# Performance work log

Hardware: AMD Instinct MI355X
Metric: run time of the kernel (lower is better)

## Reference

```python
import jax, jax.numpy as jnp
import numpy as np

B, T, C = 4, 2048, 1024
N_HEAD = 16
HEAD_DIM = C // N_HEAD


def setup_inputs() -> dict:
    key = jax.random.key(0)
    ks = jax.random.split(key, 5)
    s = 0.02
    return {
        "x": jax.random.normal(ks[0], (B, T, C), dtype=jnp.float32),
        "w_attn": jax.random.normal(ks[1], (C, 3 * C), dtype=jnp.float32) * s,
        "b_attn": jnp.zeros((3 * C,), dtype=jnp.float32),
        "w_proj": jax.random.normal(ks[2], (C, C), dtype=jnp.float32) * s,
        "b_proj": jnp.zeros((C,), dtype=jnp.float32),
    }


def reference(x, w_attn, b_attn, w_proj, b_proj):
    Bx, Tx, Cx = x.shape
    qkv = x @ w_attn + b_attn  # [B,T,3C]
    q, k, v = jnp.split(qkv, 3, axis=-1)
    # [B, H, T, D]
    q = q.reshape(Bx, Tx, N_HEAD, HEAD_DIM).transpose(0, 2, 1, 3)
    k = k.reshape(Bx, Tx, N_HEAD, HEAD_DIM).transpose(0, 2, 1, 3)
    v = v.reshape(Bx, Tx, N_HEAD, HEAD_DIM).transpose(0, 2, 1, 3)
    scale = 1.0 / np.sqrt(HEAD_DIM).astype(np.float32)
    att = jnp.einsum("bhqd,bhkd->bhqk", q, k) * scale  # [B,H,T,T]
    causal = jnp.tril(jnp.ones((Tx, Tx), dtype=bool))
    att = jnp.where(causal[None, None], att, jnp.float32(-jnp.inf))
    att = jax.nn.softmax(att, axis=-1)
    y = jnp.einsum("bhqk,bhkd->bhqd", att, v)  # [B,H,T,D]
    y = y.transpose(0, 2, 1, 3).reshape(Bx, Tx, Cx)
    return y @ w_proj + b_proj
```

## Files before the change

kernel.cpp:

```cpp
#include <hip/hip_runtime.h>
#include <hip/hip_bf16.h>

#define T_SEQ 2048
#define NHEAD 16
#define HDIM  64
#define CDIM  1024

typedef __attribute__((ext_vector_type(8))) short bf16x8;
typedef __attribute__((ext_vector_type(4))) short bf16x4;
typedef __attribute__((ext_vector_type(4))) float f32x4;

__device__ __forceinline__ unsigned short f2bf(float f) {
  union { __hip_bfloat16 h; unsigned short u; } c;
  c.h = __float2bfloat16(f);
  return c.u;
}

#define GLD16(g, l) __builtin_amdgcn_global_load_lds( \
  (const __attribute__((address_space(1))) void*)(g), \
  (__attribute__((address_space(3))) void*)(l), 16, 0, 0)

__global__ void prep_all(const float* __restrict__ x, const float* __restrict__ wa,
                         const float* __restrict__ wp, unsigned short* __restrict__ xb,
                         unsigned short* __restrict__ wat, unsigned short* __restrict__ wpt) {
  __shared__ float tile[32][33];
  const int bid = blockIdx.x;
  if (bid < 8192) {
    const int i = bid * 256 + threadIdx.x;
    const float4 v = ((const float4*)x)[i];
    ushort4 o;
    o.x = f2bf(v.x); o.y = f2bf(v.y); o.z = f2bf(v.z); o.w = f2bf(v.w);
    ((ushort4*)xb)[i] = o;
    return;
  }
  const float* in; unsigned short* out; int R, C, bx, by;
  if (bid < 11264) { in = wa; out = wat; R = 1024; C = 3072; bx = (bid - 8192) % 96; by = (bid - 8192) / 96; }
  else             { in = wp; out = wpt; R = 1024; C = 1024; bx = (bid - 11264) % 32; by = (bid - 11264) / 32; }
  const int tx = threadIdx.x & 31, ty = threadIdx.x >> 5;
  const int c0 = bx * 32, r0 = by * 32;
#pragma unroll
  for (int i = 0; i < 32; i += 8)
    tile[ty + i][tx] = in[(size_t)(r0 + ty + i) * C + c0 + tx];
  __syncthreads();
#pragma unroll
  for (int i = 0; i < 32; i += 8)
    out[(size_t)(c0 + ty + i) * R + r0 + tx] = f2bf(tile[tx][ty + i]);
}

template<int OUTF32>
__global__ __launch_bounds__(256, 2)
void gemm_bt(const unsigned short* __restrict__ A, const unsigned short* __restrict__ BT,
             const float* __restrict__ bias, void* __restrict__ outp,
             int M, int N, int K) {
  const int tid = threadIdx.x;
  const int w = tid >> 6, lane = tid & 63;
  const int lg = lane >> 4, l15 = lane & 15;
  const int wr = w >> 1, wc = w & 1;

  const int nb = gridDim.x * gridDim.y;
  const int fid = blockIdx.y * gridDim.x + blockIdx.x;
  const int swz = (fid & 7) * (nb >> 3) + (fid >> 3);
  const int n0 = (swz % gridDim.x) * 128, m0 = (swz / gridDim.x) * 128;

  __shared__ unsigned short As[128 * 64];
  __shared__ unsigned short Bs[128 * 64];

  f32x4 acc[4][4] = {};

  for (int k0 = 0; k0 < K; k0 += 64) {
    __syncthreads();
#pragma unroll
    for (int i = 0; i < 4; ++i) {
      const int cb = i * 256 + w * 64;
      const int c  = cb + lane;
      const int row = c >> 3, s = c & 7;
      const int sg = s ^ (row & 7);
      GLD16(A  + (size_t)(m0 + row) * K + k0 + sg * 8, (char*)As + cb * 16);
      GLD16(BT + (size_t)(n0 + row) * K + k0 + sg * 8, (char*)Bs + cb * 16);
    }
    __syncthreads();
#pragma unroll
    for (int ks = 0; ks < 2; ++ks) {
      bf16x8 af[4], bfr[4];
#pragma unroll
      for (int mt = 0; mt < 4; ++mt) {
        const int row = wr * 64 + mt * 16 + l15;
        af[mt] = *(const bf16x8*)&As[row * 64 + (((ks * 4 + lg) ^ (l15 & 7)) << 3)];
      }
#pragma unroll
      for (int nt = 0; nt < 4; ++nt) {
        const int row = wc * 64 + nt * 16 + l15;
        bfr[nt] = *(const bf16x8*)&Bs[row * 64 + (((ks * 4 + lg) ^ (l15 & 7)) << 3)];
      }
#pragma unroll
      for (int mt = 0; mt < 4; ++mt)
#pragma unroll
        for (int nt = 0; nt < 4; ++nt)
          acc[mt][nt] = __builtin_amdgcn_mfma_f32_16x16x32_bf16(af[mt], bfr[nt], acc[mt][nt], 0, 0, 0);
    }
  }

#pragma unroll
  for (int mt = 0; mt < 4; ++mt) {
#pragma unroll
    for (int nt = 0; nt < 4; ++nt) {
      const int col = n0 + wc * 64 + nt * 16 + l15;
      const float bv = bias[col];
#pragma unroll
      for (int j = 0; j < 4; ++j) {
        const int row = m0 + wr * 64 + mt * 16 + lg * 4 + j;
        const float v = acc[mt][nt][j] + bv;
        if (OUTF32) ((float*)outp)[(size_t)row * N + col] = v;
        else ((unsigned short*)outp)[(size_t)row * N + col] = f2bf(v);
      }
    }
  }
}

#define EXPC 0.18033688f
__global__ __launch_bounds__(512, 4)
void attn_causal5(const unsigned short* __restrict__ qkv, unsigned short* __restrict__ att) {
  const int tid = threadIdx.x;
  const int w = tid >> 6, lane = tid & 63;
  const int lg = lane >> 4, l15 = lane & 15;

  const int fid = blockIdx.x;
  const int f2 = (fid & 7) * 64 + (fid >> 3);
  const int pair = f2 & 7, bh = f2 >> 3;
  const int b = bh >> 4, h = bh & 15;

  __shared__ unsigned short Kl[2][2][64][32];
  __shared__ unsigned short Vt[2][64][64];

  const unsigned short* base = qkv + (size_t)b * T_SEQ * 3072;

  auto STAGE_K = [&](int kv0, int buf) {
    const int c = tid;
    const int kc = c >> 8, slot = (c >> 2) & 63;
    const int s2 = (c & 3) ^ ((slot >> 1) & 3);
    const int v = (slot & 35) | ((slot & 8) << 1) | ((slot & 4) << 1) | ((slot & 16) >> 2);
    GLD16(base + (size_t)(kv0 + v) * 3072 + 1024 + h * 64 + kc * 32 + s2 * 8,
          (char*)&Kl[buf][0][0][0] + w * 1024);
  };

  bf16x4 vra, vrb;
  const int vkp = tid >> 4, vd4 = tid & 15;
  auto VLOAD = [&](int kv0) {
    const unsigned short* p = base + (size_t)(kv0 + 2 * vkp) * 3072 + 2048 + h * 64 + vd4 * 4;
    vra = *(const bf16x4*)p;
    vrb = *(const bf16x4*)(p + 3072);
  };
  auto VWRITE = [&](int buf) {
    const int ch = vkp >> 2, cl = (vkp & 3) * 2;
#pragma unroll
    for (int j = 0; j < 4; ++j) {
      const int r = vd4 * 4 + j;
      const unsigned int u = (unsigned short)vra[j] |
                             ((unsigned int)(unsigned short)vrb[j] << 16);
      *(unsigned int*)&Vt[buf][r][((ch ^ (r >> 3) ^ (r & 7)) << 3) + cl] = u;
    }
  };

  bf16x8 ones;
#pragma unroll
  for (int j = 0; j < 8; ++j) ones[j] = (short)0x3F80;

  for (int half = 0; half < 2; ++half) {
    const int qt = half ? (15 - pair) : pair;
    const int q0 = qt << 7;
    const int ntl = (qt + 1) << 1;
    const int qminS = __builtin_amdgcn_readfirstlane(q0 + w * 16);
    const int qme = qminS + l15;

    bf16x8 qf[2];
#pragma unroll
    for (int kc = 0; kc < 2; ++kc)
      qf[kc] = *(const bf16x8*)(base + (size_t)qme * 3072 + h * 64 + kc * 32 + lg * 8);

    f32x4 oacc[4] = {};
    f32x4 lsum = {};
    float m = -1e30f;

    STAGE_K(0, 0);
    VLOAD(0);
    VWRITE(0);
    __syncthreads();

    for (int t = 0; t < ntl; ++t) {
      const int cur = t & 1, nxt = cur ^ 1;
      const bool pf = (t + 1) < ntl;
      if (pf) { STAGE_K((t + 1) << 6, nxt); VLOAD((t + 1) << 6); }
      const int kv0 = t << 6;

      if (kv0 <= qminS + 15) {
        const int ksl = (lg ^ ((l15 >> 1) & 3)) * 8;
        f32x4 sc[4];
        __builtin_amdgcn_s_setprio(1);
#pragma unroll
        for (int kg = 0; kg < 4; ++kg) {
          f32x4 s = {};
#pragma unroll
          for (int kc = 0; kc < 2; ++kc) {
            bf16x8 kf = *(const bf16x8*)&Kl[cur][kc][kg * 16 + l15][ksl];
            s = __builtin_amdgcn_mfma_f32_16x16x32_bf16(kf, qf[kc], s, 0, 0, 0);
          }
          sc[kg] = s;
        }
        __builtin_amdgcn_s_setprio(0);

        float sv[4][4];
        if (kv0 + 63 > qminS) {
#pragma unroll
          for (int kg = 0; kg < 4; ++kg) {
            const int colb = kv0 + ((kg >> 1) << 5) + ((kg & 1) << 2) + lg * 8;
#pragma unroll
            for (int j = 0; j < 4; ++j)
              sv[kg][j] = (colb + j <= qme) ? sc[kg][j] : -1e30f;
          }
        } else {
#pragma unroll
          for (int kg = 0; kg < 4; ++kg)
#pragma unroll
            for (int j = 0; j < 4; ++j) sv[kg][j] = sc[kg][j];
        }

        float mx = -1e30f;
#pragma unroll
        for (int kg = 0; kg < 4; ++kg) {
          const float a = fmaxf(sv[kg][0], sv[kg][1]);
          const float c2 = fmaxf(sv[kg][2], sv[kg][3]);
          mx = fmaxf(mx, fmaxf(a, c2));
        }

        if (__any(mx > m + 55.4f)) {
          float mw = fmaxf(mx, __shfl_xor(mx, 16));
          mw = fmaxf(mw, __shfl_xor(mw, 32));
          const float mnew = fmaxf(m, mw);
          const float alc = exp2f((m - mnew) * EXPC);
          m = mnew;
          float alq[4];
#pragma unroll
          for (int j = 0; j < 4; ++j)
            alq[j] = __shfl(alc, (lane & 48) | (lg * 4 + j));
#pragma unroll
          for (int j = 0; j < 4; ++j) {
            lsum[j] *= alq[j];
#pragma unroll
            for (int dt = 0; dt < 4; ++dt) oacc[dt][j] *= alq[j];
          }
        }

        const float mc = m * EXPC;
        bf16x8 pa[2];
#pragma unroll
        for (int kg = 0; kg < 4; ++kg) {
          const int ks = kg >> 1, off = (kg & 1) * 4;
#pragma unroll
          for (int j = 0; j < 4; ++j) {
            const float p = exp2f(__fmaf_rn(sv[kg][j], EXPC, -mc));
            pa[ks][off + j] = (short)f2bf(p);
          }
        }

        __builtin_amdgcn_s_setprio(1);
        lsum = __builtin_amdgcn_mfma_f32_16x16x32_bf16(pa[0], ones, lsum, 0, 0, 0);
        lsum = __builtin_amdgcn_mfma_f32_16x16x32_bf16(pa[1], ones, lsum, 0, 0, 0);
#pragma unroll
        for (int dt = 0; dt < 4; ++dt) {
          f32x4 o = oacc[dt];
          const int d = dt * 16 + l15;
          const int gx = (d >> 3) ^ (d & 7);
#pragma unroll
          for (int ks = 0; ks < 2; ++ks) {
            bf16x8 vb = *(const bf16x8*)&Vt[cur][d][((ks * 4 + lg) ^ gx) << 3];
            o = __builtin_amdgcn_mfma_f32_16x16x32_bf16(pa[ks], vb, o, 0, 0, 0);
          }
          oacc[dt] = o;
        }
        __builtin_amdgcn_s_setprio(0);
      }

      if (pf) VWRITE(nxt);
      __syncthreads();
    }

    f32x4 inv;
#pragma unroll
    for (int j = 0; j < 4; ++j) inv[j] = __builtin_amdgcn_rcpf(lsum[j]);
#pragma unroll
    for (int dt = 0; dt < 4; ++dt)
#pragma unroll
      for (int j = 0; j < 4; ++j) {
        const int q = qminS + lg * 4 + j;
        att[(size_t)(b * T_SEQ + q) * CDIM + h * HDIM + dt * 16 + l15] =
            f2bf(oacc[dt][j] * inv[j]);
      }
  }
}

extern "C" void kernel_launch(void* const* d_in, const int* in_sizes, int n_in,
                              void* d_out, int out_size, void* d_ws, size_t ws_size,
                              hipStream_t stream) {
  const float* x      = (const float*)d_in[0];
  const float* w_attn = (const float*)d_in[1];
  const float* b_attn = (const float*)d_in[2];
  const float* w_proj = (const float*)d_in[3];
  const float* b_proj = (const float*)d_in[4];

  char* ws = (char*)d_ws;
  unsigned short* xb  = (unsigned short*)(ws + 0);
  unsigned short* wat = (unsigned short*)(ws + 16777216);
  unsigned short* wpt = (unsigned short*)(ws + 23068672);
  unsigned short* qkv = (unsigned short*)(ws + 25165824);
  unsigned short* att = (unsigned short*)(ws + 75497472);

  prep_all<<<dim3(12288), 256, 0, stream>>>(x, w_attn, w_proj, xb, wat, wpt);
  gemm_bt<0><<<dim3(24, 64), 256, 0, stream>>>(xb, wat, b_attn, (void*)qkv, 8192, 3072, 1024);
  attn_causal5<<<dim3(512), 512, 0, stream>>>(qkv, att);
  gemm_bt<1><<<dim3(8, 64), 256, 0, stream>>>(att, wpt, b_proj, d_out, 8192, 1024, 1024);
}
```

Before: 172.4 us.

## Fuse x-to-bf16 conversion into QKV GEMM and process both causal tiles together

The separate pass that converted x from fp32 to bf16 is removed. The QKV GEMM now reads fp32 activations directly, converts them in registers and stores them into the swizzled LDS tile, so the intermediate bf16 buffer is never written or read back. The attention kernel now walks the KV sequence once for both its low and high query tiles, reusing each staged K/V block for two sets of MFMAs instead of running two separate passes. The cost is that A-tile loading moves from async global-to-LDS copies to synchronous register loads with twice the bytes, and the attention kernel needs more registers for two sets of accumulators.

```diff
diff --git a/kernel.cpp b/kernel.cpp
--- a/kernel.cpp
+++ b/kernel.cpp
@@ -20,22 +20,13 @@
   (const __attribute__((address_space(1))) void*)(g), \
   (__attribute__((address_space(3))) void*)(l), 16, 0, 0)
 
-__global__ void prep_all(const float* __restrict__ x, const float* __restrict__ wa,
-                         const float* __restrict__ wp, unsigned short* __restrict__ xb,
+__global__ void prep_all(const float* __restrict__ wa, const float* __restrict__ wp,
                          unsigned short* __restrict__ wat, unsigned short* __restrict__ wpt) {
   __shared__ float tile[32][33];
   const int bid = blockIdx.x;
-  if (bid < 8192) {
-    const int i = bid * 256 + threadIdx.x;
-    const float4 v = ((const float4*)x)[i];
-    ushort4 o;
-    o.x = f2bf(v.x); o.y = f2bf(v.y); o.z = f2bf(v.z); o.w = f2bf(v.w);
-    ((ushort4*)xb)[i] = o;
-    return;
-  }
   const float* in; unsigned short* out; int R, C, bx, by;
-  if (bid < 11264) { in = wa; out = wat; R = 1024; C = 3072; bx = (bid - 8192) % 96; by = (bid - 8192) / 96; }
-  else             { in = wp; out = wpt; R = 1024; C = 1024; bx = (bid - 11264) % 32; by = (bid - 11264) / 32; }
+  if (bid < 3072) { in = wa; out = wat; R = 1024; C = 3072; bx = bid % 96; by = bid / 96; }
+  else            { in = wp; out = wpt; R = 1024; C = 1024; bx = (bid - 3072) % 32; by = (bid - 3072) / 32; }
   const int tx = threadIdx.x & 31, ty = threadIdx.x >> 5;
   const int c0 = bx * 32, r0 = by * 32;
 #pragma unroll
@@ -47,9 +38,9 @@
     out[(size_t)(c0 + ty + i) * R + r0 + tx] = f2bf(tile[tx][ty + i]);
 }
 
-template<int OUTF32>
+template<int OUTF32, int AF32>
 __global__ __launch_bounds__(256, 2)
-void gemm_bt(const unsigned short* __restrict__ A, const unsigned short* __restrict__ BT,
+void gemm_bt(const void* __restrict__ Ap, const unsigned short* __restrict__ BT,
              const float* __restrict__ bias, void* __restrict__ outp,
              int M, int N, int K) {
   const int tid = threadIdx.x;
@@ -75,7 +66,21 @@
       const int c  = cb + lane;
       const int row = c >> 3, s = c & 7;
       const int sg = s ^ (row & 7);
-      GLD16(A  + (size_t)(m0 + row) * K + k0 + sg * 8, (char*)As + cb * 16);
+      if (AF32) {
+        const float* A32 = (const float*)Ap;
+        const float* p = A32 + (size_t)(m0 + row) * K + k0 + sg * 8;
+        const float4 f0 = *(const float4*)p;
+        const float4 f1 = *(const float4*)(p + 4);
+        bf16x8 pk;
+        pk[0] = (short)f2bf(f0.x); pk[1] = (short)f2bf(f0.y);
+        pk[2] = (short)f2bf(f0.z); pk[3] = (short)f2bf(f0.w);
+        pk[4] = (short)f2bf(f1.x); pk[5] = (short)f2bf(f1.y);
+        pk[6] = (short)f2bf(f1.z); pk[7] = (short)f2bf(f1.w);
+        *(bf16x8*)&As[row * 64 + s * 8] = pk;
+      } else {
+        const unsigned short* A16 = (const unsigned short*)Ap;
+        GLD16(A16 + (size_t)(m0 + row) * K + k0 + sg * 8, (char*)As + cb * 16);
+      }
       GLD16(BT + (size_t)(n0 + row) * K + k0 + sg * 8, (char*)Bs + cb * 16);
     }
     __syncthreads();
@@ -119,7 +124,7 @@
 
 #define EXPC 0.18033688f
 __global__ __launch_bounds__(512, 4)
-void attn_causal5(const unsigned short* __restrict__ qkv, unsigned short* __restrict__ att) {
+void attn_causal11(const unsigned short* __restrict__ qkv, unsigned short* __restrict__ att) {
   const int tid = threadIdx.x;
   const int w = tid >> 6, lane = tid & 63;
   const int lg = lane >> 4, l15 = lane & 15;
@@ -128,6 +133,7 @@
   const int f2 = (fid & 7) * 64 + (fid >> 3);
   const int pair = f2 & 7, bh = f2 >> 3;
   const int b = bh >> 4, h = bh & 15;
+  const int lo = pair, hi = 15 - pair;
 
   __shared__ unsigned short Kl[2][2][64][32];
   __shared__ unsigned short Vt[2][64][64];
@@ -165,135 +171,220 @@
 #pragma unroll
   for (int j = 0; j < 8; ++j) ones[j] = (short)0x3F80;
 
-  for (int half = 0; half < 2; ++half) {
-    const int qt = half ? (15 - pair) : pair;
-    const int q0 = qt << 7;
-    const int ntl = (qt + 1) << 1;
-    const int qminS = __builtin_amdgcn_readfirstlane(q0 + w * 16);
-    const int qme = qminS + l15;
-
-    bf16x8 qf[2];
-#pragma unroll
-    for (int kc = 0; kc < 2; ++kc)
-      qf[kc] = *(const bf16x8*)(base + (size_t)qme * 3072 + h * 64 + kc * 32 + lg * 8);
-
-    f32x4 oacc[4] = {};
-    f32x4 lsum = {};
-    float m = -1e30f;
-
-    STAGE_K(0, 0);
-    VLOAD(0);
-    VWRITE(0);
+  const int ntl = (hi + 1) << 1;
+  const int qminA = __builtin_amdgcn_readfirstlane(lo * 128 + w * 16);
+  const int qminB = __builtin_amdgcn_readfirstlane(hi * 128 + w * 16);
+  const int qmeA = qminA + l15, qmeB = qminB + l15;
+
+  bf16x8 qfA[2], qfB[2];
+#pragma unroll
+  for (int kc = 0; kc < 2; ++kc) {
+    qfA[kc] = *(const bf16x8*)(base + (size_t)qmeA * 3072 + h * 64 + kc * 32 + lg * 8);
+    qfB[kc] = *(const bf16x8*)(base + (size_t)qmeB * 3072 + h * 64 + kc * 32 + lg * 8);
+  }
+
+  f32x4 oaccA[4] = {}, oaccB[4] = {};
+  f32x4 lsumA = {}, lsumB = {};
+  float mA = -1e30f, mB = -1e30f;
+  bf16x8 paA[2], paB[2];
+
+  STAGE_K(0, 0);
+  VLOAD(0);
+  VWRITE(0);
+  __syncthreads();
+
+  for (int t = 0; t < ntl; ++t) {
+    const int cur = t & 1, nxt = cur ^ 1;
+    const bool pf = (t + 1) < ntl;
+    if (pf) { STAGE_K((t + 1) << 6, nxt); VLOAD((t + 1) << 6); }
+    const int kv0 = t << 6;
+    const bool actA = kv0 <= qminA + 15;
+    const bool actB = kv0 <= qminB + 15;
+
+    const int ksl = (lg ^ ((l15 >> 1) & 3)) * 8;
+    f32x4 scA[4], scB[4];
+
+    if (actA) {
+      __builtin_amdgcn_s_setprio(1);
+#pragma unroll
+      for (int kg = 0; kg < 4; ++kg) {
+        f32x4 sa = {}, sb = {};
+#pragma unroll
+        for (int kc = 0; kc < 2; ++kc) {
+          bf16x8 kf = *(const bf16x8*)&Kl[cur][kc][kg * 16 + l15][ksl];
+          sa = __builtin_amdgcn_mfma_f32_16x16x32_bf16(kf, qfA[kc], sa, 0, 0, 0);
+          sb = __builtin_amdgcn_mfma_f32_16x16x32_bf16(kf, qfB[kc], sb, 0, 0, 0);
+        }
+        scA[kg] = sa; scB[kg] = sb;
+      }
+      __builtin_amdgcn_s_setprio(0);
+    } else if (actB) {
+      __builtin_amdgcn_s_setprio(1);
+#pragma unroll
+      for (int kg = 0; kg < 4; ++kg) {
+        f32x4 sb = {};
+#pragma unroll
+        for (int kc = 0; kc < 2; ++kc) {
+          bf16x8 kf = *(const bf16x8*)&Kl[cur][kc][kg * 16 + l15][ksl];
+          sb = __builtin_amdgcn_mfma_f32_16x16x32_bf16(kf, qfB[kc], sb, 0, 0, 0);
+        }
+        scB[kg] = sb;
+      }
+      __builtin_amdgcn_s_setprio(0);
+    }
+
+    if (actA) {
+      if (kv0 + 63 > qminA) {
+#pragma unroll
+        for (int kg = 0; kg < 4; ++kg) {
+          const int colb = kv0 + ((kg >> 1) << 5) + ((kg & 1) << 2) + lg * 8;
+#pragma unroll
+          for (int j = 0; j < 4; ++j)
+            if (colb + j > qmeA) scA[kg][j] = -1e30f;
+        }
+      }
+      float mx = -1e30f;
+#pragma unroll
+      for (int kg = 0; kg < 4; ++kg) {
+        const float a = fmaxf(scA[kg][0], scA[kg][1]);
+        const float c2 = fmaxf(scA[kg][2], scA[kg][3]);
+        mx = fmaxf(mx, fmaxf(a, c2));
+      }
+      if (__any(mx > mA + 55.4f)) {
+        float mw = fmaxf(mx, __shfl_xor(mx, 16));
+        mw = fmaxf(mw, __shfl_xor(mw, 32));
+        const float mnew = fmaxf(mA, mw);
+        const float alc = exp2f((mA - mnew) * EXPC);
+        mA = mnew;
+        float alq[4];
+#pragma unroll
+        for (int j = 0; j < 4; ++j)
+          alq[j] = __shfl(alc, (lane & 48) | (lg * 4 + j));
+#pragma unroll
+        for (int j = 0; j < 4; ++j) {
+          lsumA[j] *= alq[j];
+#pragma unroll
+          for (int dt = 0; dt < 4; ++dt) oaccA[dt][j] *= alq[j];
+        }
+      }
+      const float mc = mA * EXPC;
+#pragma unroll
+      for (int kg = 0; kg < 4; ++kg) {
+        const int ks = kg >> 1, off = (kg & 1) * 4;
+#pragma unroll
+        for (int j = 0; j < 4; ++j) {
+          const float p = exp2f(__fmaf_rn(scA[kg][j], EXPC, -mc));
+          paA[ks][off + j] = (short)f2bf(p);
+        }
+      }
+    }
+
+    if (actB) {
+      if (kv0 + 63 > qminB) {
+#pragma unroll
+        for (int kg = 0; kg < 4; ++kg) {
+          const int colb = kv0 + ((kg >> 1) << 5) + ((kg & 1) << 2) + lg * 8;
+#pragma unroll
+          for (int j = 0; j < 4; ++j)
+            if (colb + j > qmeB) scB[kg][j] = -1e30f;
+        }
+      }
+      float mx = -1e30f;
+#pragma unroll
+      for (int kg = 0; kg < 4; ++kg) {
+        const float a = fmaxf(scB[kg][0], scB[kg][1]);
+        const float c2 = fmaxf(scB[kg][2], scB[kg][3]);
+        mx = fmaxf(mx, fmaxf(a, c2));
+      }
+      if (__any(mx > mB + 55.4f)) {
+        float mw = fmaxf(mx, __shfl_xor(mx, 16));
+        mw = fmaxf(mw, __shfl_xor(mw, 32));
+        const float mnew = fmaxf(mB, mw);
+        const float alc = exp2f((mB - mnew) * EXPC);
+        mB = mnew;
+        float alq[4];
+#pragma unroll
+        for (int j = 0; j < 4; ++j)
+          alq[j] = __shfl(alc, (lane & 48) | (lg * 4 + j));
+#pragma unroll
+        for (int j = 0; j < 4; ++j) {
+          lsumB[j] *= alq[j];
+#pragma unroll
+          for (int dt = 0; dt < 4; ++dt) oaccB[dt][j] *= alq[j];
+        }
+      }
+      const float mc = mB * EXPC;
+#pragma unroll
+      for (int kg = 0; kg < 4; ++kg) {
+        const int ks = kg >> 1, off = (kg & 1) * 4;
+#pragma unroll
+        for (int j = 0; j < 4; ++j) {
+          const float p = exp2f(__fmaf_rn(scB[kg][j], EXPC, -mc));
+          paB[ks][off + j] = (short)f2bf(p);
+        }
+      }
+    }
+
+    if (actA) {
+      __builtin_amdgcn_s_setprio(1);
+      lsumA = __builtin_amdgcn_mfma_f32_16x16x32_bf16(paA[0], ones, lsumA, 0, 0, 0);
+      lsumA = __builtin_amdgcn_mfma_f32_16x16x32_bf16(paA[1], ones, lsumA, 0, 0, 0);
+      lsumB = __builtin_amdgcn_mfma_f32_16x16x32_bf16(paB[0], ones, lsumB, 0, 0, 0);
+      lsumB = __builtin_amdgcn_mfma_f32_16x16x32_bf16(paB[1], ones, lsumB, 0, 0, 0);
+#pragma unroll
+      for (int dt = 0; dt < 4; ++dt) {
+        f32x4 oa = oaccA[dt], ob = oaccB[dt];
+        const int d = dt * 16 + l15;
+        const int gx = (d >> 3) ^ (d & 7);
+#pragma unroll
+        for (int ks = 0; ks < 2; ++ks) {
+          bf16x8 vb = *(const bf16x8*)&Vt[cur][d][((ks * 4 + lg) ^ gx) << 3];
+          oa = __builtin_amdgcn_mfma_f32_16x16x32_bf16(paA[ks], vb, oa, 0, 0, 0);
+          ob = __builtin_amdgcn_mfma_f32_16x16x32_bf16(paB[ks], vb, ob, 0, 0, 0);
+        }
+        oaccA[dt] = oa; oaccB[dt] = ob;
+      }
+      __builtin_amdgcn_s_setprio(0);
+    } else if (actB) {
+      __builtin_amdgcn_s_setprio(1);
+      lsumB = __builtin_amdgcn_mfma_f32_16x16x32_bf16(paB[0], ones, lsumB, 0, 0, 0);
+      lsumB = __builtin_amdgcn_mfma_f32_16x16x32_bf16(paB[1], ones, lsumB, 0, 0, 0);
+#pragma unroll
+      for (int dt = 0; dt < 4; ++dt) {
+        f32x4 ob = oaccB[dt];
+        const int d = dt * 16 + l15;
+        const int gx = (d >> 3) ^ (d & 7);
+#pragma unroll
+        for (int ks = 0; ks < 2; ++ks) {
+          bf16x8 vb = *(const bf16x8*)&Vt[cur][d][((ks * 4 + lg) ^ gx) << 3];
+          ob = __builtin_amdgcn_mfma_f32_16x16x32_bf16(paB[ks], vb, ob, 0, 0, 0);
+        }
+        oaccB[dt] = ob;
+      }
+      __builtin_amdgcn_s_setprio(0);
+    }
+
+    if (pf) VWRITE(nxt);
     __syncthreads();
-
-    for (int t = 0; t < ntl; ++t) {
-      const int cur = t & 1, nxt = cur ^ 1;
-      const bool pf = (t + 1) < ntl;
-      if (pf) { STAGE_K((t + 1) << 6, nxt); VLOAD((t + 1) << 6); }
-      const int kv0 = t << 6;
-
-      if (kv0 <= qminS + 15) {
-        const int ksl = (lg ^ ((l15 >> 1) & 3)) * 8;
-        f32x4 sc[4];
-        __builtin_amdgcn_s_setprio(1);
-#pragma unroll
-        for (int kg = 0; kg < 4; ++kg) {
-          f32x4 s = {};
-#pragma unroll
-          for (int kc = 0; kc < 2; ++kc) {
-            bf16x8 kf = *(const bf16x8*)&Kl[cur][kc][kg * 16 + l15][ksl];
-            s = __builtin_amdgcn_mfma_f32_16x16x32_bf16(kf, qf[kc], s, 0, 0, 0);
-          }
-          sc[kg] = s;
-        }
-        __builtin_amdgcn_s_setprio(0);
-
-        float sv[4][4];
-        if (kv0 + 63 > qminS) {
-#pragma unroll
-          for (int kg = 0; kg < 4; ++kg) {
-            const int colb = kv0 + ((kg >> 1) << 5) + ((kg & 1) << 2) + lg * 8;
-#pragma unroll
-            for (int j = 0; j < 4; ++j)
-              sv[kg][j] = (colb + j <= qme) ? sc[kg][j] : -1e30f;
-          }
-        } else {
-#pragma unroll
-          for (int kg = 0; kg < 4; ++kg)
-#pragma unroll
-            for (int j = 0; j < 4; ++j) sv[kg][j] = sc[kg][j];
-        }
-
-        float mx = -1e30f;
-#pragma unroll
-        for (int kg = 0; kg < 4; ++kg) {
-          const float a = fmaxf(sv[kg][0], sv[kg][1]);
-          const float c2 = fmaxf(sv[kg][2], sv[kg][3]);
-          mx = fmaxf(mx, fmaxf(a, c2));
-        }
-
-        if (__any(mx > m + 55.4f)) {
-          float mw = fmaxf(mx, __shfl_xor(mx, 16));
-          mw = fmaxf(mw, __shfl_xor(mw, 32));
-          const float mnew = fmaxf(m, mw);
-          const float alc = exp2f((m - mnew) * EXPC);
-          m = mnew;
-          float alq[4];
-#pragma unroll
-          for (int j = 0; j < 4; ++j)
-            alq[j] = __shfl(alc, (lane & 48) | (lg * 4 + j));
-#pragma unroll
-          for (int j = 0; j < 4; ++j) {
-            lsum[j] *= alq[j];
-#pragma unroll
-            for (int dt = 0; dt < 4; ++dt) oacc[dt][j] *= alq[j];
-          }
-        }
-
-        const float mc = m * EXPC;
-        bf16x8 pa[2];
-#pragma unroll
-        for (int kg = 0; kg < 4; ++kg) {
-          const int ks = kg >> 1, off = (kg & 1) * 4;
-#pragma unroll
-          for (int j = 0; j < 4; ++j) {
-            const float p = exp2f(__fmaf_rn(sv[kg][j], EXPC, -mc));
-            pa[ks][off + j] = (short)f2bf(p);
-          }
-        }
-
-        __builtin_amdgcn_s_setprio(1);
-        lsum = __builtin_amdgcn_mfma_f32_16x16x32_bf16(pa[0], ones, lsum, 0, 0, 0);
-        lsum = __builtin_amdgcn_mfma_f32_16x16x32_bf16(pa[1], ones, lsum, 0, 0, 0);
-#pragma unroll
-        for (int dt = 0; dt < 4; ++dt) {
-          f32x4 o = oacc[dt];
-          const int d = dt * 16 + l15;
-          const int gx = (d >> 3) ^ (d & 7);
-#pragma unroll
-          for (int ks = 0; ks < 2; ++ks) {
-            bf16x8 vb = *(const bf16x8*)&Vt[cur][d][((ks * 4 + lg) ^ gx) << 3];
-            o = __builtin_amdgcn_mfma_f32_16x16x32_bf16(pa[ks], vb, o, 0, 0, 0);
-          }
-          oacc[dt] = o;
-        }
-        __builtin_amdgcn_s_setprio(0);
-      }
-
-      if (pf) VWRITE(nxt);
-      __syncthreads();
-    }
-
-    f32x4 inv;
-#pragma unroll
-    for (int j = 0; j < 4; ++j) inv[j] = __builtin_amdgcn_rcpf(lsum[j]);
+  }
+
+  {
+    f32x4 invA, invB;
+#pragma unroll
+    for (int j = 0; j < 4; ++j) {
+      invA[j] = __builtin_amdgcn_rcpf(lsumA[j]);
+      invB[j] = __builtin_amdgcn_rcpf(lsumB[j]);
+    }
 #pragma unroll
     for (int dt = 0; dt < 4; ++dt)
 #pragma unroll
       for (int j = 0; j < 4; ++j) {
-        const int q = qminS + lg * 4 + j;
-        att[(size_t)(b * T_SEQ + q) * CDIM + h * HDIM + dt * 16 + l15] =
-            f2bf(oacc[dt][j] * inv[j]);
+        const int qa = qminA + lg * 4 + j;
+        const int qb = qminB + lg * 4 + j;
+        att[(size_t)(b * T_SEQ + qa) * CDIM + h * HDIM + dt * 16 + l15] =
+            f2bf(oaccA[dt][j] * invA[j]);
+        att[(size_t)(b * T_SEQ + qb) * CDIM + h * HDIM + dt * 16 + l15] =
+            f2bf(oaccB[dt][j] * invB[j]);
       }
   }
 }
@@ -308,14 +399,13 @@
   const float* b_proj = (const float*)d_in[4];
 
   char* ws = (char*)d_ws;
-  unsigned short* xb  = (unsigned short*)(ws + 0);
   unsigned short* wat = (unsigned short*)(ws + 16777216);
   unsigned short* wpt = (unsigned short*)(ws + 23068672);
   unsigned short* qkv = (unsigned short*)(ws + 25165824);
   unsigned short* att = (unsigned short*)(ws + 75497472);
 
-  prep_all<<<dim3(12288), 256, 0, stream>>>(x, w_attn, w_proj, xb, wat, wpt);
-  gemm_bt<0><<<dim3(24, 64), 256, 0, stream>>>(xb, wat, b_attn, (void*)qkv, 8192, 3072, 1024);
-  attn_causal5<<<dim3(512), 512, 0, stream>>>(qkv, att);
-  gemm_bt<1><<<dim3(8, 64), 256, 0, stream>>>(att, wpt, b_proj, d_out, 8192, 1024, 1024);
+  prep_all<<<dim3(4096), 256, 0, stream>>>(w_attn, w_proj, wat, wpt);
+  gemm_bt<0, 1><<<dim3(24, 64), 256, 0, stream>>>((const void*)x, wat, b_attn, (void*)qkv, 8192, 3072, 1024);
+  attn_causal11<<<dim3(512), 512, 0, stream>>>(qkv, att);
+  gemm_bt<1, 0><<<dim3(8, 64), 256, 0, stream>>>((const void*)att, wpt, b_proj, d_out, 8192, 1024, 1024);
 }
```

Result: slower. 366.1 us (+112.4%).

## Triple-buffer K/V tiles in causal attention with two-deep prefetch and manual waitcnt

Applied to the files above, without the earlier changes.

The attention kernel moves from double to triple buffering of the K and V LDS tiles, prefetching two tiles ahead. The loop is unrolled by two with rotating buffer indices, and __syncthreads is replaced by explicit s_waitcnt vmcnt(3) plus s_barrier, so the next tile's loads can stay in flight across the barrier. This aims to hide global load latency behind MFMA compute, at the cost of 50% more LDS per block and extra V staging registers, which may lower occupancy.

```diff
diff --git a/kernel.cpp b/kernel.cpp
--- a/kernel.cpp
+++ b/kernel.cpp
@@ -119,7 +119,7 @@
 
 #define EXPC 0.18033688f
 __global__ __launch_bounds__(512, 4)
-void attn_causal5(const unsigned short* __restrict__ qkv, unsigned short* __restrict__ att) {
+void attn_causal12(const unsigned short* __restrict__ qkv, unsigned short* __restrict__ att) {
   const int tid = threadIdx.x;
   const int w = tid >> 6, lane = tid & 63;
   const int lg = lane >> 4, l15 = lane & 15;
@@ -129,8 +129,8 @@
   const int pair = f2 & 7, bh = f2 >> 3;
   const int b = bh >> 4, h = bh & 15;
 
-  __shared__ unsigned short Kl[2][2][64][32];
-  __shared__ unsigned short Vt[2][64][64];
+  __shared__ unsigned short Kl[3][2][64][32];
+  __shared__ unsigned short Vt[3][64][64];
 
   const unsigned short* base = qkv + (size_t)b * T_SEQ * 3072;
 
@@ -143,20 +143,19 @@
           (char*)&Kl[buf][0][0][0] + w * 1024);
   };
 
-  bf16x4 vra, vrb;
   const int vkp = tid >> 4, vd4 = tid & 15;
-  auto VLOAD = [&](int kv0) {
+  auto VLOAD = [&](int kv0, bf16x4& ra, bf16x4& rb) {
     const unsigned short* p = base + (size_t)(kv0 + 2 * vkp) * 3072 + 2048 + h * 64 + vd4 * 4;
-    vra = *(const bf16x4*)p;
-    vrb = *(const bf16x4*)(p + 3072);
+    ra = *(const bf16x4*)p;
+    rb = *(const bf16x4*)(p + 3072);
   };
-  auto VWRITE = [&](int buf) {
+  auto VWRITE = [&](int buf, bf16x4 ra, bf16x4 rb) {
     const int ch = vkp >> 2, cl = (vkp & 3) * 2;
 #pragma unroll
     for (int j = 0; j < 4; ++j) {
       const int r = vd4 * 4 + j;
-      const unsigned int u = (unsigned short)vra[j] |
-                             ((unsigned int)(unsigned short)vrb[j] << 16);
+      const unsigned int u = (unsigned short)ra[j] |
+                             ((unsigned int)(unsigned short)rb[j] << 16);
       *(unsigned int*)&Vt[buf][r][((ch ^ (r >> 3) ^ (r & 7)) << 3) + cl] = u;
     }
   };
@@ -180,108 +179,130 @@
     f32x4 oacc[4] = {};
     f32x4 lsum = {};
     float m = -1e30f;
+    bf16x4 v0a, v0b, v1a, v1b;
+
+    auto COMPUTE = [&](int t, int bA) {
+      const int kv0 = t << 6;
+      if (kv0 > qminS + 15) return;
+      const int ksl = (lg ^ ((l15 >> 1) & 3)) * 8;
+      f32x4 sc[4];
+      __builtin_amdgcn_s_setprio(1);
+#pragma unroll
+      for (int kg = 0; kg < 4; ++kg) {
+        f32x4 s = {};
+#pragma unroll
+        for (int kc = 0; kc < 2; ++kc) {
+          bf16x8 kf = *(const bf16x8*)&Kl[bA][kc][kg * 16 + l15][ksl];
+          s = __builtin_amdgcn_mfma_f32_16x16x32_bf16(kf, qf[kc], s, 0, 0, 0);
+        }
+        sc[kg] = s;
+      }
+      __builtin_amdgcn_s_setprio(0);
+
+      float sv[4][4];
+      if (kv0 + 63 > qminS) {
+#pragma unroll
+        for (int kg = 0; kg < 4; ++kg) {
+          const int colb = kv0 + ((kg >> 1) << 5) + ((kg & 1) << 2) + lg * 8;
+#pragma unroll
+          for (int j = 0; j < 4; ++j)
+            sv[kg][j] = (colb + j <= qme) ? sc[kg][j] : -1e30f;
+        }
+      } else {
+#pragma unroll
+        for (int kg = 0; kg < 4; ++kg)
+#pragma unroll
+          for (int j = 0; j < 4; ++j) sv[kg][j] = sc[kg][j];
+      }
+
+      float mx = -1e30f;
+#pragma unroll
+      for (int kg = 0; kg < 4; ++kg) {
+        const float a = fmaxf(sv[kg][0], sv[kg][1]);
+        const float c2 = fmaxf(sv[kg][2], sv[kg][3]);
+        mx = fmaxf(mx, fmaxf(a, c2));
+      }
+
+      if (__any(mx > m + 55.4f)) {
+        float mw = fmaxf(mx, __shfl_xor(mx, 16));
+        mw = fmaxf(mw, __shfl_xor(mw, 32));
+        const float mnew = fmaxf(m, mw);
+        const float alc = exp2f((m - mnew) * EXPC);
+        m = mnew;
+        float alq[4];
+#pragma unroll
+        for (int j = 0; j < 4; ++j)
+          alq[j] = __shfl(alc, (lane & 48) | (lg * 4 + j));
+#pragma unroll
+        for (int j = 0; j < 4; ++j) {
+          lsum[j] *= alq[j];
+#pragma unroll
+          for (int dt = 0; dt < 4; ++dt) oacc[dt][j] *= alq[j];
+        }
+      }
+
+      const float mc = m * EXPC;
+      bf16x8 pa[2];
+#pragma unroll
+      for (int kg = 0; kg < 4; ++kg) {
+        const int ks = kg >> 1, off = (kg & 1) * 4;
+#pragma unroll
+        for (int j = 0; j < 4; ++j) {
+          const float p = exp2f(__fmaf_rn(sv[kg][j], EXPC, -mc));
+          pa[ks][off + j] = (short)f2bf(p);
+        }
+      }
+
+      __builtin_amdgcn_s_setprio(1);
+      lsum = __builtin_amdgcn_mfma_f32_16x16x32_bf16(pa[0], ones, lsum, 0, 0, 0);
+      lsum = __builtin_amdgcn_mfma_f32_16x16x32_bf16(pa[1], ones, lsum, 0, 0, 0);
+#pragma unroll
+      for (int dt = 0; dt < 4; ++dt) {
+        f32x4 o = oacc[dt];
+        const int d = dt * 16 + l15;
+        const int gx = (d >> 3) ^ (d & 7);
+#pragma unroll
+        for (int ks = 0; ks < 2; ++ks) {
+          bf16x8 vb = *(const bf16x8*)&Vt[bA][d][((ks * 4 + lg) ^ gx) << 3];
+          o = __builtin_amdgcn_mfma_f32_16x16x32_bf16(pa[ks], vb, o, 0, 0, 0);
+        }
+        oacc[dt] = o;
+      }
+      __builtin_amdgcn_s_setprio(0);
+    };
+
+    auto TAIL = [&](int t, int bB, bf16x4 wa, bf16x4 wb) {
+      if ((t + 1) < ntl) VWRITE(bB, wa, wb);
+      if ((t + 2) < ntl) {
+        asm volatile("s_waitcnt vmcnt(3) lgkmcnt(0)" ::: "memory");
+      } else {
+        asm volatile("s_waitcnt vmcnt(0) lgkmcnt(0)" ::: "memory");
+      }
+      __builtin_amdgcn_sched_barrier(0);
+      __builtin_amdgcn_s_barrier();
+      __builtin_amdgcn_sched_barrier(0);
+    };
 
     STAGE_K(0, 0);
-    VLOAD(0);
-    VWRITE(0);
-    __syncthreads();
-
-    for (int t = 0; t < ntl; ++t) {
-      const int cur = t & 1, nxt = cur ^ 1;
-      const bool pf = (t + 1) < ntl;
-      if (pf) { STAGE_K((t + 1) << 6, nxt); VLOAD((t + 1) << 6); }
-      const int kv0 = t << 6;
-
-      if (kv0 <= qminS + 15) {
-        const int ksl = (lg ^ ((l15 >> 1) & 3)) * 8;
-        f32x4 sc[4];
-        __builtin_amdgcn_s_setprio(1);
-#pragma unroll
-        for (int kg = 0; kg < 4; ++kg) {
-          f32x4 s = {};
-#pragma unroll
-          for (int kc = 0; kc < 2; ++kc) {
-            bf16x8 kf = *(const bf16x8*)&Kl[cur][kc][kg * 16 + l15][ksl];
-            s = __builtin_amdgcn_mfma_f32_16x16x32_bf16(kf, qf[kc], s, 0, 0, 0);
-          }
-          sc[kg] = s;
-        }
-        __builtin_amdgcn_s_setprio(0);
-
-        float sv[4][4];
-        if (kv0 + 63 > qminS) {
-#pragma unroll
-          for (int kg = 0; kg < 4; ++kg) {
-            const int colb = kv0 + ((kg >> 1) << 5) + ((kg & 1) << 2) + lg * 8;
-#pragma unroll
-            for (int j = 0; j < 4; ++j)
-              sv[kg][j] = (colb + j <= qme) ? sc[kg][j] : -1e30f;
-          }
-        } else {
-#pragma unroll
-          for (int kg = 0; kg < 4; ++kg)
-#pragma unroll
-            for (int j = 0; j < 4; ++j) sv[kg][j] = sc[kg][j];
-        }
-
-        float mx = -1e30f;
-#pragma unroll
-        for (int kg = 0; kg < 4; ++kg) {
-          const float a = fmaxf(sv[kg][0], sv[kg][1]);
-          const float c2 = fmaxf(sv[kg][2], sv[kg][3]);
-          mx = fmaxf(mx, fmaxf(a, c2));
-        }
-
-        if (__any(mx > m + 55.4f)) {
-          float mw = fmaxf(mx, __shfl_xor(mx, 16));
-          mw = fmaxf(mw, __shfl_xor(mw, 32));
-          const float mnew = fmaxf(m, mw);
-          const float alc = exp2f((m - mnew) * EXPC);
-          m = mnew;
-          float alq[4];
-#pragma unroll
-          for (int j = 0; j < 4; ++j)
-            alq[j] = __shfl(alc, (lane & 48) | (lg * 4 + j));
-#pragma unroll
-          for (int j = 0; j < 4; ++j) {
-            lsum[j] *= alq[j];
-#pragma unroll
-            for (int dt = 0; dt < 4; ++dt) oacc[dt][j] *= alq[j];
-          }
-        }
-
-        const float mc = m * EXPC;
-        bf16x8 pa[2];
-#pragma unroll
-        for (int kg = 0; kg < 4; ++kg) {
-          const int ks = kg >> 1, off = (kg & 1) * 4;
-#pragma unroll
-          for (int j = 0; j < 4; ++j) {
-            const float p = exp2f(__fmaf_rn(sv[kg][j], EXPC, -mc));
-            pa[ks][off + j] = (short)f2bf(p);
-          }
-        }
-
-        __builtin_amdgcn_s_setprio(1);
-        lsum = __builtin_amdgcn_mfma_f32_16x16x32_bf16(pa[0], ones, lsum, 0, 0, 0);
-        lsum = __builtin_amdgcn_mfma_f32_16x16x32_bf16(pa[1], ones, lsum, 0, 0, 0);
-#pragma unroll
-        for (int dt = 0; dt < 4; ++dt) {
-          f32x4 o = oacc[dt];
-          const int d = dt * 16 + l15;
-          const int gx = (d >> 3) ^ (d & 7);
-#pragma unroll
-          for (int ks = 0; ks < 2; ++ks) {
-            bf16x8 vb = *(const bf16x8*)&Vt[cur][d][((ks * 4 + lg) ^ gx) << 3];
-            o = __builtin_amdgcn_mfma_f32_16x16x32_bf16(pa[ks], vb, o, 0, 0, 0);
-          }
-          oacc[dt] = o;
-        }
-        __builtin_amdgcn_s_setprio(0);
-      }
-
-      if (pf) VWRITE(nxt);
-      __syncthreads();
+    VLOAD(0, v0a, v0b);
+    VWRITE(0, v0a, v0b);
+    STAGE_K(64, 1);
+    VLOAD(64, v1a, v1b);
+    asm volatile("s_waitcnt vmcnt(3) lgkmcnt(0)" ::: "memory");
+    __builtin_amdgcn_sched_barrier(0);
+    __builtin_amdgcn_s_barrier();
+    __builtin_amdgcn_sched_barrier(0);
+
+    int bA = 0, bB = 1, bC = 2;
+    for (int t = 0; t < ntl; t += 2) {
+      if ((t + 2) < ntl) { STAGE_K((t + 2) << 6, bC); VLOAD((t + 2) << 6, v0a, v0b); }
+      COMPUTE(t, bA);
+      TAIL(t, bB, v1a, v1b);
+      if ((t + 3) < ntl) { STAGE_K((t + 3) << 6, bA); VLOAD((t + 3) << 6, v1a, v1b); }
+      COMPUTE(t + 1, bB);
+      TAIL(t + 1, bC, v0a, v0b);
+      const int nA = bC, nB2 = bA, nC = bB;
+      bA = nA; bB = nB2; bC = nC;
     }
 
     f32x4 inv;
@@ -316,6 +337,6 @@
 
   prep_all<<<dim3(12288), 256, 0, stream>>>(x, w_attn, w_proj, xb, wat, wpt);
   gemm_bt<0><<<dim3(24, 64), 256, 0, stream>>>(xb, wat, b_attn, (void*)qkv, 8192, 3072, 1024);
-  attn_causal5<<<dim3(512), 512, 0, stream>>>(qkv, att);
+  attn_causal12<<<dim3(512), 512, 0, stream>>>(qkv, att);
   gemm_bt<1><<<dim3(8, 64), 256, 0, stream>>>(att, wpt, b_proj, d_out, 8192, 1024, 1024);
 }
```

Result: no change. 173.4 us, median of 2 (+0.6%).
